# Performance work log

Measured on AMD Instinct MI355X. Metric: run time of the kernel, lower is better.

## Reference

```python
import jax, jax.numpy as jnp
import numpy as np


def _cdist(x, y):
    # Euclidean (p=2) pairwise distances, matching torch.cdist.
    # x: [B, N, D], y: [B, M, D] -> [B, N, M]
    xx = jnp.sum(x * x, axis=-1)                      # [B, N]
    yy = jnp.sum(y * y, axis=-1)                      # [B, M]
    zz = jnp.einsum('bnd,bmd->bnm', x, y)             # [B, N, M]
    d2 = xx[:, :, None] + yy[:, None, :] - 2.0 * zz
    return jnp.sqrt(jnp.maximum(d2, 0.0))


def setup_inputs() -> dict:
    key = jax.random.key(0)
    k1, k2 = jax.random.split(key)
    gts = jax.random.normal(k1, (4, 8192, 3), dtype=jnp.float32)
    preds = jax.random.normal(k2, (4, 8192, 3), dtype=jnp.float32)
    return {"gts": gts, "preds": preds}


def reference(gts, preds):
    P = _cdist(gts, preds)                 # [B, N, M]
    loss_1 = jnp.sum(jnp.min(P, axis=1), axis=1)  # min over gts points, sum over preds
    loss_2 = jnp.sum(jnp.min(P, axis=2), axis=1)  # min over preds points, sum over gts
    return loss_1 + loss_2                 # [B]
```

## Files before the change

kernel.cpp:

```cpp
#include <hip/hip_runtime.h>
#include <math.h>

#define BB 4
#define NPTS 8192
#define THREADS 512
#define NQ_TOTAL (2 * BB * NPTS)
#define QBLK 512
#define QPWV 64
#define QUARTN 2048
#define NFRAG (QUARTN / 32)
#define FBLK 512

typedef __attribute__((ext_vector_type(4)))  short bf16x4;
typedef __attribute__((ext_vector_type(16))) float f32x16;


__device__ __forceinline__ unsigned short f2bf(float f) {
    unsigned u = __float_as_uint(f);
    u += 0x7FFF + ((u >> 16) & 1);
    return (unsigned short)(u >> 16);
}
__device__ __forceinline__ float bf2f(unsigned short h) {
    return __uint_as_float(((unsigned)h) << 16);
}

__global__ __launch_bounds__(256) void pack_kernel(
    const float* __restrict__ gts, const float* __restrict__ preds,
    uint2* __restrict__ refpl, uint2* __restrict__ qpl,
    unsigned* __restrict__ minpart, float* __restrict__ out) {
    int idx = blockIdx.x * 256 + threadIdx.x;
    if (idx < BB) out[idx] = 0.0f;
    if (idx >= NQ_TOTAL) return;
    minpart[idx] = 0x7F7FFFFFu;
    int set  = idx / (BB * NPTS);
    int pidx = idx - set * (BB * NPTS);
    const float* src = set ? preds : gts;
    unsigned short hx = f2bf(src[pidx * 3 + 0]);
    unsigned short hy = f2bf(src[pidx * 3 + 1]);
    unsigned short hz = f2bf(src[pidx * 3 + 2]);
    float fx = bf2f(hx), fy = bf2f(hy), fz = bf2f(hz);
    float rr = fmaf(fx, fx, fmaf(fy, fy, fz * fz));
    unsigned short hrr = f2bf(rr);
    unsigned short hlo = f2bf(rr - bf2f(hrr));
    const unsigned short ONE = 0x3F80;

    uint2 rlo, rhi;
    rlo.x = (unsigned)hx  | ((unsigned)hy  << 16);
    rlo.y = (unsigned)hz  | ((unsigned)hrr << 16);
    rhi.x = (unsigned)hlo | ((unsigned)ONE << 16);
    rhi.y = (unsigned)ONE;
    refpl[idx]            = rlo;
    refpl[NQ_TOTAL + idx] = rhi;

    unsigned short nx = f2bf(-2.0f * fx);
    unsigned short ny = f2bf(-2.0f * fy);
    unsigned short nz = f2bf(-2.0f * fz);
    uint2 qlo, qhi;
    qlo.x = (unsigned)nx  | ((unsigned)ny  << 16);
    qlo.y = (unsigned)nz  | ((unsigned)ONE << 16);
    qhi.x = (unsigned)ONE | ((unsigned)hrr << 16);
    qhi.y = (unsigned)hlo;
    qpl[idx]            = qlo;
    qpl[NQ_TOTAL + idx] = qhi;
}

#define FOLD8(P, X0, X1, X2, X3)                                   \
    X0 = fminf(fminf((P)[0],  (P)[1]),  X0);                       \
    X1 = fminf(fminf((P)[2],  (P)[3]),  X1);                       \
    X2 = fminf(fminf((P)[4],  (P)[5]),  X2);                       \
    X3 = fminf(fminf((P)[6],  (P)[7]),  X3);                       \
    X0 = fminf(fminf((P)[8],  (P)[9]),  X0);                       \
    X1 = fminf(fminf((P)[10], (P)[11]), X1);                       \
    X2 = fminf(fminf((P)[12], (P)[13]), X2);                       \
    X3 = fminf(fminf((P)[14], (P)[15]), X3);

#define MFMA8(A, B, C) __builtin_amdgcn_mfma_f32_32x32x8bf16_1k(A, B, C, 0, 0, 0)

#define STEP(AQ, FN, DO_LOAD)                                               \
    {                                                                       \
        f32x16 d0 = MFMA8(AQ, bq0, zc);                                     \
        f32x16 d1 = MFMA8(AQ, bq1, zc);                                     \
        if (DO_LOAD) AQ = spv[poff + (FN) * 32 + l31];                      \
        FOLD8(d0, c0, c1, c2, c3);                                          \
        FOLD8(d1, c4, c5, c6, c7);                                          \
    }

#define STAGE()                                                             \
    _Pragma("unroll")                                                       \
    for (int i = 0; i < 2; ++i) {                                           \
        __builtin_amdgcn_global_load_lds(                                   \
            (const unsigned*)(rlo_src + i * 1024 + wid * 128 + lane * 2),   \
            (unsigned*)&sref[0][i * 1024 + wid * 128], 16, 0, 0);           \
        __builtin_amdgcn_global_load_lds(                                   \
            (const unsigned*)(rhi_src + i * 1024 + wid * 128 + lane * 2),   \
            (unsigned*)&sref[1][i * 1024 + wid * 128], 16, 0, 0);           \
    }

__global__ __launch_bounds__(THREADS, 4) void chamfer_kernel(
    const uint2* __restrict__ refpl, const uint2* __restrict__ qpl,
    unsigned* __restrict__ minpart) {
    __shared__ uint2 sref[2][QUARTN];

    int tid  = threadIdx.x;
    int blk  = blockIdx.x;
    int quart= blk >> 7;
    int dir  = (blk >> 6) & 1;
    int b    = (blk >> 4) & 3;
    int qg   = blk & 15;
    int rset = dir;
    int qset = dir ^ 1;
    int wid  = tid >> 6;
    int lane = tid & 63;
    int l31  = lane & 31;
    int khalf= lane >> 5;

    size_t rbase = (size_t)(rset * BB + b) * NPTS + (size_t)quart * QUARTN;
    const uint2* rlo_src = refpl + rbase;
    const uint2* rhi_src = refpl + NQ_TOTAL + rbase;

    STAGE();

    size_t qoff = (size_t)(qset * BB + b) * NPTS + (size_t)qg * QBLK
                + (size_t)wid * QPWV;
    const bf16x4* qv = (const bf16x4*)qpl;
    bf16x4 bq0 = qv[(size_t)khalf * NQ_TOTAL + qoff + l31];
    bf16x4 bq1 = qv[(size_t)khalf * NQ_TOTAL + qoff + 32 + l31];
    __syncthreads();

    f32x16 zc;
    #pragma unroll
    for (int r = 0; r < 16; ++r) zc[r] = 0.0f;

    float c0 = 3.0e38f, c1 = 3.0e38f, c2 = 3.0e38f, c3 = 3.0e38f;
    float c4 = 3.0e38f, c5 = 3.0e38f, c6 = 3.0e38f, c7 = 3.0e38f;

    const bf16x4* spv = (const bf16x4*)sref;
    const int poff = khalf * QUARTN;

    bf16x4 a0 = spv[poff + 0 * 32 + l31];
    bf16x4 a1 = spv[poff + 1 * 32 + l31];
    bf16x4 a2 = spv[poff + 2 * 32 + l31];
    bf16x4 a3 = spv[poff + 3 * 32 + l31];

    #pragma unroll
    for (int m = 0; m < NFRAG / 4; ++m) {
        const bool L = (m < NFRAG / 4 - 1);
        STEP(a0, (m + 1) * 4 + 0, L);
        STEP(a1, (m + 1) * 4 + 1, L);
        STEP(a2, (m + 1) * 4 + 2, L);
        STEP(a3, (m + 1) * 4 + 3, L);
    }

    float m0 = fminf(fminf(c0, c1), fminf(c2, c3));
    m0 = fminf(m0, __shfl_xor(m0, 32, 64));
    float m1 = fminf(fminf(c4, c5), fminf(c6, c7));
    m1 = fminf(m1, __shfl_xor(m1, 32, 64));

    size_t qid = (size_t)(dir * BB + b) * NPTS + (size_t)qg * QBLK
               + (size_t)wid * QPWV;
    if (lane < 32) {
        atomicMin(minpart + qid + l31,      __float_as_uint(fmaxf(m0, 0.0f)));
        atomicMin(minpart + qid + 32 + l31, __float_as_uint(fmaxf(m1, 0.0f)));
    }
}

__global__ __launch_bounds__(256) void merge_kernel(
    const unsigned* __restrict__ minpart, float* __restrict__ out) {
    int t  = blockIdx.x * 256 + threadIdx.x;
    uint4 v = ((const uint4*)minpart)[t];
    float d = sqrtf(__uint_as_float(v.x)) + sqrtf(__uint_as_float(v.y))
            + sqrtf(__uint_as_float(v.z)) + sqrtf(__uint_as_float(v.w));
    int b = (blockIdx.x >> 3) & 3;

    #pragma unroll
    for (int off = 32; off > 0; off >>= 1)
        d += __shfl_down(d, off, 64);

    __shared__ float wsum[4];
    int lane = threadIdx.x & 63;
    int wid  = threadIdx.x >> 6;
    if (lane == 0) wsum[wid] = d;
    __syncthreads();
    if (threadIdx.x == 0)
        atomicAdd(out + b, wsum[0] + wsum[1] + wsum[2] + wsum[3]);
}

extern "C" void kernel_launch(void* const* d_in, const int* in_sizes, int n_in,
                              void* d_out, int out_size, void* d_ws, size_t ws_size,
                              hipStream_t stream) {
    const float* gts   = (const float*)d_in[0];
    const float* preds = (const float*)d_in[1];
    float* out = (float*)d_out;

    char* ws = (char*)d_ws;
    uint2*    refpl   = (uint2*)ws;
    uint2*    qpl     = (uint2*)(ws + (size_t)NQ_TOTAL * 16);
    unsigned* minpart = (unsigned*)(ws + (size_t)NQ_TOTAL * 32);

    pack_kernel<<<NQ_TOTAL / 256, 256, 0, stream>>>(
        gts, preds, refpl, qpl, minpart, out);

    chamfer_kernel<<<FBLK, THREADS, 0, stream>>>(refpl, qpl, minpart);

    merge_kernel<<<NQ_TOTAL / 4 / 256, 256, 0, stream>>>(minpart, out);
}
```

Measured before the change: 71.47 us.

## Fuse bf16 point packing into chamfer kernel and replace atomicMin with per-quarter partials

Removes the separate pack kernel. Each chamfer block now reads raw float xyz, converts it to the bf16 hi/lo operand layout and writes the reference tile straight into LDS. The query fragments are built in registers. Instead of atomicMin on a pre-initialised buffer, each reference quarter writes its own partial minima, and the merge kernel takes the min over the four partials before the sqrt and sum. This drops one kernel launch, the workspace round trip and the atomics, in exchange for redundant packing work across blocks and uncoalesced strided loads of query coordinates.

```diff
diff --git a/kernel.cpp b/kernel.cpp
--- a/kernel.cpp
+++ b/kernel.cpp
@@ -24,45 +24,38 @@
     return __uint_as_float(((unsigned)h) << 16);
 }
 
-__global__ __launch_bounds__(256) void pack_kernel(
-    const float* __restrict__ gts, const float* __restrict__ preds,
-    uint2* __restrict__ refpl, uint2* __restrict__ qpl,
-    unsigned* __restrict__ minpart, float* __restrict__ out) {
-    int idx = blockIdx.x * 256 + threadIdx.x;
-    if (idx < BB) out[idx] = 0.0f;
-    if (idx >= NQ_TOTAL) return;
-    minpart[idx] = 0x7F7FFFFFu;
-    int set  = idx / (BB * NPTS);
-    int pidx = idx - set * (BB * NPTS);
-    const float* src = set ? preds : gts;
-    unsigned short hx = f2bf(src[pidx * 3 + 0]);
-    unsigned short hy = f2bf(src[pidx * 3 + 1]);
-    unsigned short hz = f2bf(src[pidx * 3 + 2]);
-    float fx = bf2f(hx), fy = bf2f(hy), fz = bf2f(hz);
-    float rr = fmaf(fx, fx, fmaf(fy, fy, fz * fz));
-    unsigned short hrr = f2bf(rr);
-    unsigned short hlo = f2bf(rr - bf2f(hrr));
-    const unsigned short ONE = 0x3F80;
-
-    uint2 rlo, rhi;
-    rlo.x = (unsigned)hx  | ((unsigned)hy  << 16);
-    rlo.y = (unsigned)hz  | ((unsigned)hrr << 16);
-    rhi.x = (unsigned)hlo | ((unsigned)ONE << 16);
-    rhi.y = (unsigned)ONE;
-    refpl[idx]            = rlo;
-    refpl[NQ_TOTAL + idx] = rhi;
-
-    unsigned short nx = f2bf(-2.0f * fx);
-    unsigned short ny = f2bf(-2.0f * fy);
-    unsigned short nz = f2bf(-2.0f * fz);
-    uint2 qlo, qhi;
-    qlo.x = (unsigned)nx  | ((unsigned)ny  << 16);
-    qlo.y = (unsigned)nz  | ((unsigned)ONE << 16);
-    qhi.x = (unsigned)ONE | ((unsigned)hrr << 16);
-    qhi.y = (unsigned)hlo;
-    qpl[idx]            = qlo;
-    qpl[NQ_TOTAL + idx] = qhi;
-}
+#define ONE16 ((unsigned short)0x3F80)
+
+#define PACKR(X, Y, Z, LO, HI)                                              \
+    {                                                                       \
+        unsigned short hx = f2bf(X), hy = f2bf(Y), hz = f2bf(Z);            \
+        float fx = bf2f(hx), fy = bf2f(hy), fz = bf2f(hz);                  \
+        float rr = fmaf(fx, fx, fmaf(fy, fy, fz * fz));                     \
+        unsigned short hrr = f2bf(rr), hlo = f2bf(rr - bf2f(hrr));          \
+        (LO).x = (unsigned)hx  | ((unsigned)hy  << 16);                     \
+        (LO).y = (unsigned)hz  | ((unsigned)hrr << 16);                     \
+        (HI).x = (unsigned)hlo | ((unsigned)ONE16 << 16);                   \
+        (HI).y = (unsigned)ONE16;                                           \
+    }
+
+#define PACKQ(X, Y, Z, BQ)                                                  \
+    {                                                                       \
+        unsigned short hx = f2bf(X), hy = f2bf(Y), hz = f2bf(Z);            \
+        float fx = bf2f(hx), fy = bf2f(hy), fz = bf2f(hz);                  \
+        float qq = fmaf(fx, fx, fmaf(fy, fy, fz * fz));                     \
+        unsigned short hq = f2bf(qq), hql = f2bf(qq - bf2f(hq));            \
+        if (khalf == 0) {                                                   \
+            (BQ)[0] = (short)f2bf(-2.0f * fx);                              \
+            (BQ)[1] = (short)f2bf(-2.0f * fy);                              \
+            (BQ)[2] = (short)f2bf(-2.0f * fz);                              \
+            (BQ)[3] = (short)ONE16;                                         \
+        } else {                                                            \
+            (BQ)[0] = (short)ONE16;                                         \
+            (BQ)[1] = (short)hq;                                            \
+            (BQ)[2] = (short)hql;                                           \
+            (BQ)[3] = 0;                                                    \
+        }                                                                   \
+    }
 
 #define FOLD8(P, X0, X1, X2, X3)                                   \
     X0 = fminf(fminf((P)[0],  (P)[1]),  X0);                       \
@@ -85,20 +78,9 @@
         FOLD8(d1, c4, c5, c6, c7);                                          \
     }
 
-#define STAGE()                                                             \
-    _Pragma("unroll")                                                       \
-    for (int i = 0; i < 2; ++i) {                                           \
-        __builtin_amdgcn_global_load_lds(                                   \
-            (const unsigned*)(rlo_src + i * 1024 + wid * 128 + lane * 2),   \
-            (unsigned*)&sref[0][i * 1024 + wid * 128], 16, 0, 0);           \
-        __builtin_amdgcn_global_load_lds(                                   \
-            (const unsigned*)(rhi_src + i * 1024 + wid * 128 + lane * 2),   \
-            (unsigned*)&sref[1][i * 1024 + wid * 128], 16, 0, 0);           \
-    }
-
 __global__ __launch_bounds__(THREADS, 4) void chamfer_kernel(
-    const uint2* __restrict__ refpl, const uint2* __restrict__ qpl,
-    unsigned* __restrict__ minpart) {
+    const float* __restrict__ gts, const float* __restrict__ preds,
+    float* __restrict__ minpart, float* __restrict__ out) {
     __shared__ uint2 sref[2][QUARTN];
 
     int tid  = threadIdx.x;
@@ -107,24 +89,38 @@
     int dir  = (blk >> 6) & 1;
     int b    = (blk >> 4) & 3;
     int qg   = blk & 15;
-    int rset = dir;
-    int qset = dir ^ 1;
     int wid  = tid >> 6;
     int lane = tid & 63;
     int l31  = lane & 31;
     int khalf= lane >> 5;
 
-    size_t rbase = (size_t)(rset * BB + b) * NPTS + (size_t)quart * QUARTN;
-    const uint2* rlo_src = refpl + rbase;
-    const uint2* rhi_src = refpl + NQ_TOTAL + rbase;
-
-    STAGE();
-
-    size_t qoff = (size_t)(qset * BB + b) * NPTS + (size_t)qg * QBLK
-                + (size_t)wid * QPWV;
-    const bf16x4* qv = (const bf16x4*)qpl;
-    bf16x4 bq0 = qv[(size_t)khalf * NQ_TOTAL + qoff + l31];
-    bf16x4 bq1 = qv[(size_t)khalf * NQ_TOTAL + qoff + 32 + l31];
+    if (blk == 0 && tid < BB) out[tid] = 0.0f;
+
+    const float* qsrc = (dir ^ 1) ? preds : gts;
+    size_t qpt = (size_t)b * NPTS + (size_t)qg * QBLK + (size_t)wid * QPWV + l31;
+    float qx0 = qsrc[qpt * 3],        qy0 = qsrc[qpt * 3 + 1],
+          qz0 = qsrc[qpt * 3 + 2];
+    float qx1 = qsrc[(qpt + 32) * 3], qy1 = qsrc[(qpt + 32) * 3 + 1],
+          qz1 = qsrc[(qpt + 32) * 3 + 2];
+    bf16x4 bq0, bq1;
+    PACKQ(qx0, qy0, qz0, bq0);
+    PACKQ(qx1, qy1, qz1, bq1);
+
+    const float* rsrc = dir ? preds : gts;
+    size_t rfbase = ((size_t)b * NPTS + (size_t)quart * QUARTN) * 3;
+    const float4* rf4 = (const float4*)(rsrc + rfbase);
+    float4 f0 = rf4[3 * tid], f1 = rf4[3 * tid + 1], f2 = rf4[3 * tid + 2];
+    uint2 l0, l1, l2, l3, h0, h1, h2, h3;
+    PACKR(f0.x, f0.y, f0.z, l0, h0);
+    PACKR(f0.w, f1.x, f1.y, l1, h1);
+    PACKR(f1.z, f1.w, f2.x, l2, h2);
+    PACKR(f2.y, f2.z, f2.w, l3, h3);
+    uint4* dlo = (uint4*)&sref[0][4 * tid];
+    dlo[0] = make_uint4(l0.x, l0.y, l1.x, l1.y);
+    dlo[1] = make_uint4(l2.x, l2.y, l3.x, l3.y);
+    uint4* dhi = (uint4*)&sref[1][4 * tid];
+    dhi[0] = make_uint4(h0.x, h0.y, h1.x, h1.y);
+    dhi[1] = make_uint4(h2.x, h2.y, h3.x, h3.y);
     __syncthreads();
 
     f32x16 zc;
@@ -158,19 +154,27 @@
 
     size_t qid = (size_t)(dir * BB + b) * NPTS + (size_t)qg * QBLK
                + (size_t)wid * QPWV;
+    float* mp = minpart + (size_t)quart * NQ_TOTAL + qid;
     if (lane < 32) {
-        atomicMin(minpart + qid + l31,      __float_as_uint(fmaxf(m0, 0.0f)));
-        atomicMin(minpart + qid + 32 + l31, __float_as_uint(fmaxf(m1, 0.0f)));
+        mp[l31]      = fmaxf(m0, 0.0f);
+        mp[32 + l31] = fmaxf(m1, 0.0f);
     }
 }
 
 __global__ __launch_bounds__(256) void merge_kernel(
-    const unsigned* __restrict__ minpart, float* __restrict__ out) {
-    int t  = blockIdx.x * 256 + threadIdx.x;
-    uint4 v = ((const uint4*)minpart)[t];
-    float d = sqrtf(__uint_as_float(v.x)) + sqrtf(__uint_as_float(v.y))
-            + sqrtf(__uint_as_float(v.z)) + sqrtf(__uint_as_float(v.w));
-    int b = (blockIdx.x >> 3) & 3;
+    const float* __restrict__ minpart, float* __restrict__ out) {
+    int t = blockIdx.x * 256 + threadIdx.x;
+    const float4* mp4 = (const float4*)minpart;
+    float4 v0 = mp4[t];
+    float4 v1 = mp4[t + NQ_TOTAL / 4];
+    float4 v2 = mp4[t + 2 * (NQ_TOTAL / 4)];
+    float4 v3 = mp4[t + 3 * (NQ_TOTAL / 4)];
+    float mx = fminf(fminf(v0.x, v1.x), fminf(v2.x, v3.x));
+    float my = fminf(fminf(v0.y, v1.y), fminf(v2.y, v3.y));
+    float mz = fminf(fminf(v0.z, v1.z), fminf(v2.z, v3.z));
+    float mw = fminf(fminf(v0.w, v1.w), fminf(v2.w, v3.w));
+    float d = sqrtf(mx) + sqrtf(my) + sqrtf(mz) + sqrtf(mw);
+    int b = (t >> 11) & 3;
 
     #pragma unroll
     for (int off = 32; off > 0; off >>= 1)
@@ -192,15 +196,9 @@
     const float* preds = (const float*)d_in[1];
     float* out = (float*)d_out;
 
-    char* ws = (char*)d_ws;
-    uint2*    refpl   = (uint2*)ws;
-    uint2*    qpl     = (uint2*)(ws + (size_t)NQ_TOTAL * 16);
-    unsigned* minpart = (unsigned*)(ws + (size_t)NQ_TOTAL * 32);
-
-    pack_kernel<<<NQ_TOTAL / 256, 256, 0, stream>>>(
-        gts, preds, refpl, qpl, minpart, out);
-
-    chamfer_kernel<<<FBLK, THREADS, 0, stream>>>(refpl, qpl, minpart);
+    float* minpart = (float*)d_ws;
+
+    chamfer_kernel<<<FBLK, THREADS, 0, stream>>>(gts, preds, minpart, out);
 
     merge_kernel<<<NQ_TOTAL / 4 / 256, 256, 0, stream>>>(minpart, out);
 }
```

Result: faster. 68.28 us (median of 2 runs) (-4.5%).
